# Kernel optimization log

Measured on AMD Instinct MI355X. Metric: run time of the kernel, lower is better.

## Reference

```python
import jax, jax.numpy as jnp
import numpy as np

UNITS = 256
BATCH = 256


def _make_sizes():
    rng = np.random.default_rng(0)
    nclasses = rng.integers(2, 16, size=BATCH).astype(np.int32)
    nfeature = rng.integers(50, 201, size=BATCH).astype(np.int32)
    return nclasses, nfeature


def setup_inputs() -> dict:
    key = jax.random.key(0)
    nclasses, nfeature = _make_sizes()
    total = int((nclasses.astype(np.int64) * nfeature).sum())
    x = jax.random.normal(key, (total, UNITS), dtype=jnp.float32)
    return {
        "x": x,
        "nclasses": jnp.asarray(nclasses),
        "nfeature": jnp.asarray(nfeature),
    }


def reference(x, nclasses, nfeature):
    # sizes[i] = nclasses[i] * nfeature[i]; segment i covers rows [start_i, start_i + sizes_i)
    sizes = (nclasses * nfeature).astype(jnp.int32)          # [B]
    num_segments = sizes.shape[0]
    ends = jnp.cumsum(sizes)                                  # [B]
    # segment id of each row: first segment whose end exceeds the row index
    seg_ids = jnp.searchsorted(ends, jnp.arange(x.shape[0]), side="right")
    sums = jax.ops.segment_sum(x, seg_ids, num_segments=num_segments)  # [B, units]
    return sums / sizes[:, None].astype(x.dtype)              # per-segment mean
```

## Files before the change

### kernel.cpp

```cpp
#include <hip/hip_runtime.h>

#define UNITS 256
#define BATCH 256

typedef float fx4 __attribute__((ext_vector_type(4)));

__global__ __launch_bounds__(256) void k_prep(const int* __restrict__ nclasses,
                                              const int* __restrict__ nfeature,
                                              int* __restrict__ ends,
                                              float* __restrict__ out) {
    const int t = threadIdx.x;
    const int b = blockIdx.x;
    out[b * UNITS + t] = 0.0f;
    if (b == 0) {
        __shared__ int s[BATCH];
        s[t] = nclasses[t] * nfeature[t];
        __syncthreads();
        #pragma unroll
        for (int off = 1; off < BATCH; off <<= 1) {
            int v   = s[t];
            int add = (t >= off) ? s[t - off] : 0;
            __syncthreads();
            s[t] = v + add;
            __syncthreads();
        }
        ends[t] = s[t];
    }
}

__global__ __launch_bounds__(256) void k_accum(const float* __restrict__ x,
                                               const int* __restrict__ ends,
                                               const int* __restrict__ nclasses,
                                               const int* __restrict__ nfeature,
                                               float* __restrict__ out,
                                               int total_rows, int rpb) {
    __shared__ int   s_ends[BATCH];
    __shared__ float s_inv[BATCH];
    __shared__ fx4   s_red[3][64];
    const int t  = threadIdx.x;
    const int ln = t & 63;
    const int rl = t >> 6;
    s_ends[t] = ends[t];
    s_inv[t]  = 1.0f / (float)(nclasses[t] * nfeature[t]);
    __syncthreads();

    const int c    = ln << 2;
    const int r0   = blockIdx.x * rpb;
    const int rend = min(r0 + rpb, total_rows);
    if (r0 >= total_rows) return;

    int lo = 0, hi = BATCH;
    while (lo < hi) {
        int mid = (lo + hi) >> 1;
        if (s_ends[mid] > r0) hi = mid; else lo = mid + 1;
    }
    int seg = lo;

    int r = r0 + rl;
    const float* p = x + (size_t)r * UNITS + c;

    for (;;) {
        const int stop = min(s_ends[seg], rend);
        int cnt = (stop - r + 3) >> 2;
        if (cnt < 0) cnt = 0;
        r += cnt << 2;

        fx4 acc = {0.f, 0.f, 0.f, 0.f};
        int k = 0;
        for (; k + 4 <= cnt; k += 4) {
            fx4 v0 = *(const fx4*)(p);
            fx4 v1 = *(const fx4*)(p + 4 * UNITS);
            fx4 v2 = *(const fx4*)(p + 8 * UNITS);
            fx4 v3 = *(const fx4*)(p + 12 * UNITS);
            p += 16 * UNITS;
            acc += (v0 + v1) + (v2 + v3);
        }
        for (; k < cnt; ++k) {
            fx4 v = *(const fx4*)(p);
            p += 4 * UNITS;
            acc += v;
        }

        if (rl) s_red[rl - 1][ln] = acc;
        __syncthreads();
        if (rl == 0) {
            acc += s_red[0][ln];
            acc += s_red[1][ln];
            acc += s_red[2][ln];
            const float s = s_inv[seg];
            float* o = out + seg * UNITS + c;
            unsafeAtomicAdd(o + 0, acc.x * s);
            unsafeAtomicAdd(o + 1, acc.y * s);
            unsafeAtomicAdd(o + 2, acc.z * s);
            unsafeAtomicAdd(o + 3, acc.w * s);
        }
        if (s_ends[seg] >= rend) break;
        ++seg;
        __syncthreads();
    }
}

extern "C" void kernel_launch(void* const* d_in, const int* in_sizes, int n_in,
                              void* d_out, int out_size, void* d_ws, size_t ws_size,
                              hipStream_t stream) {
    const float* x        = (const float*)d_in[0];
    const int*   nclasses = (const int*)d_in[1];
    const int*   nfeature = (const int*)d_in[2];
    float*       out      = (float*)d_out;
    int*         ends     = (int*)d_ws;

    const int total_rows = in_sizes[0] / UNITS;

    int rpb = (total_rows + 2047) / 2048;
    rpb = (rpb + 3) & ~3;
    if (rpb < 4) rpb = 4;
    const int nblocks = (total_rows + rpb - 1) / rpb;

    k_prep<<<BATCH, UNITS, 0, stream>>>(nclasses, nfeature, ends, out);
    k_accum<<<nblocks, 256, 0, stream>>>(x, ends, nclasses, nfeature, out,
                                         total_rows, rpb);
}
```

Before: 56.27 us.

## Fold prefix scan into accumulate kernel, balance rows, nontemporal unrolled loads

```diff
diff --git a/kernel.cpp b/kernel.cpp
--- a/kernel.cpp
+++ b/kernel.cpp
@@ -5,57 +5,53 @@
 
 typedef float fx4 __attribute__((ext_vector_type(4)));
 
-__global__ __launch_bounds__(256) void k_prep(const int* __restrict__ nclasses,
-                                              const int* __restrict__ nfeature,
-                                              int* __restrict__ ends,
-                                              float* __restrict__ out) {
-    const int t = threadIdx.x;
-    const int b = blockIdx.x;
-    out[b * UNITS + t] = 0.0f;
-    if (b == 0) {
-        __shared__ int s[BATCH];
-        s[t] = nclasses[t] * nfeature[t];
-        __syncthreads();
-        #pragma unroll
-        for (int off = 1; off < BATCH; off <<= 1) {
-            int v   = s[t];
-            int add = (t >= off) ? s[t - off] : 0;
-            __syncthreads();
-            s[t] = v + add;
-            __syncthreads();
-        }
-        ends[t] = s[t];
-    }
+__global__ __launch_bounds__(256) void k_zero(float* __restrict__ out) {
+    const int i = (blockIdx.x * 256 + threadIdx.x) << 2;
+    *reinterpret_cast<fx4*>(out + i) = fx4{0.f, 0.f, 0.f, 0.f};
 }
 
 __global__ __launch_bounds__(256) void k_accum(const float* __restrict__ x,
-                                               const int* __restrict__ ends,
                                                const int* __restrict__ nclasses,
                                                const int* __restrict__ nfeature,
                                                float* __restrict__ out,
-                                               int total_rows, int rpb) {
+                                               int total_rows, int lo, int nE4) {
     __shared__ int   s_ends[BATCH];
     __shared__ float s_inv[BATCH];
     __shared__ fx4   s_red[3][64];
     const int t  = threadIdx.x;
     const int ln = t & 63;
     const int rl = t >> 6;
-    s_ends[t] = ends[t];
-    s_inv[t]  = 1.0f / (float)(nclasses[t] * nfeature[t]);
+
+    {
+        const int sz = nclasses[t] * nfeature[t];
+        s_inv[t]  = 1.0f / (float)sz;
+        s_ends[t] = sz;
+    }
     __syncthreads();
+    #pragma unroll
+    for (int off = 1; off < BATCH; off <<= 1) {
+        int v   = s_ends[t];
+        int add = (t >= off) ? s_ends[t - off] : 0;
+        __syncthreads();
+        s_ends[t] = v + add;
+        __syncthreads();
+    }
 
-    const int c    = ln << 2;
-    const int r0   = blockIdx.x * rpb;
-    const int rend = min(r0 + rpb, total_rows);
-    if (r0 >= total_rows) return;
+    const int b    = blockIdx.x;
+    const int hi   = lo + 4;
+    const int r0   = (b < nE4) ? b * hi : nE4 * hi + (b - nE4) * lo;
+    const int sz   = (b < nE4) ? hi : lo;
+    const int rend = min(r0 + sz, total_rows);
+    if (r0 >= rend) return;
 
-    int lo = 0, hi = BATCH;
-    while (lo < hi) {
-        int mid = (lo + hi) >> 1;
-        if (s_ends[mid] > r0) hi = mid; else lo = mid + 1;
+    int slo = 0, shi = BATCH;
+    while (slo < shi) {
+        int mid = (slo + shi) >> 1;
+        if (s_ends[mid] > r0) shi = mid; else slo = mid + 1;
     }
-    int seg = lo;
+    int seg = slo;
 
+    const int c = ln << 2;
     int r = r0 + rl;
     const float* p = x + (size_t)r * UNITS + c;
 
@@ -67,16 +63,20 @@
 
         fx4 acc = {0.f, 0.f, 0.f, 0.f};
         int k = 0;
-        for (; k + 4 <= cnt; k += 4) {
-            fx4 v0 = *(const fx4*)(p);
-            fx4 v1 = *(const fx4*)(p + 4 * UNITS);
-            fx4 v2 = *(const fx4*)(p + 8 * UNITS);
-            fx4 v3 = *(const fx4*)(p + 12 * UNITS);
-            p += 16 * UNITS;
-            acc += (v0 + v1) + (v2 + v3);
+        for (; k + 8 <= cnt; k += 8) {
+            fx4 v0 = __builtin_nontemporal_load((const fx4*)(p));
+            fx4 v1 = __builtin_nontemporal_load((const fx4*)(p + 4  * UNITS));
+            fx4 v2 = __builtin_nontemporal_load((const fx4*)(p + 8  * UNITS));
+            fx4 v3 = __builtin_nontemporal_load((const fx4*)(p + 12 * UNITS));
+            fx4 v4 = __builtin_nontemporal_load((const fx4*)(p + 16 * UNITS));
+            fx4 v5 = __builtin_nontemporal_load((const fx4*)(p + 20 * UNITS));
+            fx4 v6 = __builtin_nontemporal_load((const fx4*)(p + 24 * UNITS));
+            fx4 v7 = __builtin_nontemporal_load((const fx4*)(p + 28 * UNITS));
+            p += 32 * UNITS;
+            acc += ((v0 + v1) + (v2 + v3)) + ((v4 + v5) + (v6 + v7));
         }
         for (; k < cnt; ++k) {
-            fx4 v = *(const fx4*)(p);
+            fx4 v = __builtin_nontemporal_load((const fx4*)(p));
             p += 4 * UNITS;
             acc += v;
         }
@@ -107,16 +107,15 @@
     const int*   nclasses = (const int*)d_in[1];
     const int*   nfeature = (const int*)d_in[2];
     float*       out      = (float*)d_out;
-    int*         ends     = (int*)d_ws;
 
     const int total_rows = in_sizes[0] / UNITS;
 
-    int rpb = (total_rows + 2047) / 2048;
-    rpb = (rpb + 3) & ~3;
-    if (rpb < 4) rpb = 4;
-    const int nblocks = (total_rows + rpb - 1) / rpb;
+    const int q   = total_rows >> 11;
+    const int lo  = q & ~3;
+    const int E   = total_rows - (lo << 11);
+    const int nE4 = (E + 3) >> 2;
 
-    k_prep<<<BATCH, UNITS, 0, stream>>>(nclasses, nfeature, ends, out);
-    k_accum<<<nblocks, 256, 0, stream>>>(x, ends, nclasses, nfeature, out,
-                                         total_rows, rpb);
+    k_zero<<<64, 256, 0, stream>>>(out);
+    k_accum<<<2048, 256, 0, stream>>>(x, nclasses, nfeature, out,
+                                      total_rows, lo, nE4);
 }
```

Result: slower. 58.13 us (+3.3%).
